# Kernel tuning notes

Measured on AMD Instinct MI355X. Metric: run time of the kernel, lower is better.

Reference implementation:

```python
import jax, jax.numpy as jnp
import numpy as np

EPS = 1e-12   # F.normalize eps
COS_EPS = 1e-8  # F.cosine_similarity eps

B, S, V, D, P, L = 4, 2048, 64, 1024, 8, 24
H = D // 24            # prefix_transform bottleneck = 42
K = 2 * L * D          # 49152 output feature dim


def setup_inputs() -> dict:
    key = jax.random.key(0)
    ks = jax.random.split(key, 8)
    return {
        "prefix": jax.random.randint(ks[0], (B, V), 0, V),
        "ctx_embeds": jax.random.normal(ks[1], (B, S, D), jnp.float32),
        "tables": jax.random.normal(ks[2], (P, V, D), jnp.float32) * 0.02,
        "lora_prefix_emb": jax.random.normal(ks[3], (P, D), jnp.float32),
        "w1": jax.random.normal(ks[4], (D, H), jnp.float32) * 0.02,
        "b1": jnp.zeros((H,), jnp.float32),
        "w2": jax.random.normal(ks[5], (H, K), jnp.float32) * 0.02,
        "b2": jnp.zeros((K,), jnp.float32),
    }


def _gates(ctx_embeds, lora_prefix_emb):
    """select_prefix, vectorized over the num_prefix_set loop.

    The original builds sim_i = bmm(norm(emb), norm(e_i.repeat(B,S,1), dim=0).permute)
    of shape [B,S,S]; since the key is repeated, every column of sim is identical,
    so we carry the column vector [P,B,S] and the math is exact.
    """
    b, s, _ = ctx_embeds.shape
    # normalize embedding over feature dim (F.normalize p=2 dim=2)
    emb_n = ctx_embeds / jnp.maximum(
        jnp.linalg.norm(ctx_embeds, axis=2, keepdims=True), EPS)
    # F.normalize over dim=0 of a tensor repeated B times -> sign(x)/sqrt(B)
    u = lora_prefix_emb / jnp.maximum(
        jnp.sqrt(float(b)) * jnp.abs(lora_prefix_emb), EPS)  # [P,D]
    v = jnp.einsum('bsd,pd->pbs', emb_n, u)          # column of sim matrix
    c = jnp.maximum(v, 0.0)                          # clamp(min=0)
    # F.normalize over last dim (length S, all entries equal c) -> c/(sqrt(S)*c)
    n = c / jnp.maximum(jnp.sqrt(float(s)) * c, EPS)
    w = jax.nn.softmax(n, axis=2)                    # softmax over token dim (dim=1 in torch layout)
    a_v = jnp.einsum('pbs,bsd->pbd', w, ctx_embeds)  # attended value per expert
    e_norm = jnp.linalg.norm(lora_prefix_emb, axis=1)          # [P]
    a_norm = jnp.linalg.norm(a_v, axis=2)                      # [P,B]
    cos = jnp.einsum('pd,pbd->pb', lora_prefix_emb, a_v) / \
        jnp.maximum(e_norm[:, None] * a_norm, COS_EPS)
    return jax.nn.softmax(cos.T, axis=-1)            # self.s_t, [B,P]


def reference(prefix, ctx_embeds, tables, lora_prefix_emb, w1, b1, w2, b2):
    s_t = _gates(ctx_embeds, lora_prefix_emb)        # [B,P]
    # forward() re-applies softmax to self.s_t (faithful double softmax)
    gate = jax.nn.softmax(s_t, axis=-1)              # [B,P]
    tok = tables[:, prefix]                          # [P,B,V,D] per-expert embedding lookup
    h = jnp.tanh(jnp.einsum('pbvd,dh->pbvh', tok, w1) + b1)
    pkv = jnp.einsum('pbvh,hk->pbvk', h, w2) + b2    # [P,B,V,K]
    out = jnp.einsum('bp,pbvk->bvk', gate, pkv)      # gated mixture over experts
    return out
```

## Files before the change

### kernel.cpp

```cpp
#include <hip/hip_runtime.h>

#define BB 4
#define SS 2048
#define VV 64
#define DD 1024
#define PP 8
#define HH 42
#define KK 49152

static constexpr float F_EPS = 1e-12f;
static constexpr float ALPHA = 1.02234304f;

__global__ __launch_bounds__(512) void kU_fused(
    const float* __restrict__ ctx, const float* __restrict__ lora,
    const float* __restrict__ tables, const float* __restrict__ w1,
    const float* __restrict__ b1, float* __restrict__ part,
    float* __restrict__ h_all) {
  __shared__ float smem[PP * DD + 16 + 32 * PP];
  const int t = threadIdx.x;
  const int b = blockIdx.y;
  if (blockIdx.x < 64) {
    const int chunk = blockIdx.x;
    float* u_lds = smem;
    float* w_lds = smem + PP * DD + 16;
    for (int i = t; i < PP * DD; i += 512) {
      float e = lora[i];
      u_lds[i] = e / fmaxf(2.0f * fabsf(e), F_EPS);
    }
    __syncthreads();
    const int wave = t >> 6, lane = t & 63;
    const int rbase = b * SS + chunk * 32 + wave * 4;
    const float4* ctx4 = (const float4*)ctx;
    const float4* u4 = (const float4*)u_lds;
    float dot[4][PP];
    #pragma unroll
    for (int i = 0; i < 4; ++i)
      #pragma unroll
      for (int p = 0; p < PP; ++p) dot[i][p] = 0.f;
    #pragma unroll
    for (int j = 0; j < 4; ++j) {
      float4 c[4];
      #pragma unroll
      for (int i = 0; i < 4; ++i)
        c[i] = ctx4[(size_t)(rbase + i) * 256 + j * 64 + lane];
      #pragma unroll
      for (int p = 0; p < PP; ++p) {
        float4 u = u4[p * 256 + j * 64 + lane];
        #pragma unroll
        for (int i = 0; i < 4; ++i)
          dot[i][p] += c[i].x * u.x + c[i].y * u.y + c[i].z * u.z + c[i].w * u.w;
      }
    }
    const int sel = lane & 7;
    #pragma unroll
    for (int i = 0; i < 4; ++i) {
      float d0 = dot[i][0], d1 = dot[i][1], d2 = dot[i][2], d3 = dot[i][3];
      float d4 = dot[i][4], d5 = dot[i][5], d6 = dot[i][6], d7 = dot[i][7];
      #pragma unroll
      for (int m = 1; m <= 4; m <<= 1) {
        d0 += __shfl_xor(d0, m, 64); d1 += __shfl_xor(d1, m, 64);
        d2 += __shfl_xor(d2, m, 64); d3 += __shfl_xor(d3, m, 64);
        d4 += __shfl_xor(d4, m, 64); d5 += __shfl_xor(d5, m, 64);
        d6 += __shfl_xor(d6, m, 64); d7 += __shfl_xor(d7, m, 64);
      }
      float v = d0;
      v = (sel == 1) ? d1 : v; v = (sel == 2) ? d2 : v;
      v = (sel == 3) ? d3 : v; v = (sel == 4) ? d4 : v;
      v = (sel == 5) ? d5 : v; v = (sel == 6) ? d6 : v;
      v = (sel == 7) ? d7 : v;
      v += __shfl_xor(v, 8, 64);
      v += __shfl_xor(v, 16, 64);
      v += __shfl_xor(v, 32, 64);
      if (lane < PP)
        w_lds[(wave * 4 + i) * PP + lane] = (v > 0.0f) ? ALPHA : 1.0f;
    }
    __syncthreads();
    float2 acc[PP];
    #pragma unroll
    for (int p = 0; p < PP; ++p) acc[p] = make_float2(0.f, 0.f);
    const float2* ctx2 = (const float2*)ctx;
    const float4* w4 = (const float4*)w_lds;
    #pragma unroll 4
    for (int sl = 0; sl < 32; ++sl) {
      float2 c = ctx2[(size_t)(b * SS + chunk * 32 + sl) * 512 + t];
      float4 wa = w4[sl * 2];
      float4 wb = w4[sl * 2 + 1];
      float w[PP] = {wa.x, wa.y, wa.z, wa.w, wb.x, wb.y, wb.z, wb.w};
      #pragma unroll
      for (int p = 0; p < PP; ++p) {
        acc[p].x += w[p] * c.x;
        acc[p].y += w[p] * c.y;
      }
    }
    float2* part2 = (float2*)part;
    #pragma unroll
    for (int p = 0; p < PP; ++p)
      part2[(size_t)((b * 64 + chunk) * PP + p) * 512 + t] = acc[p];
  } else {
    float* row_lds = smem;
    float* partial = smem + DD;
    const int r = (blockIdx.x - 64) * 4 + b;
    ((float2*)row_lds)[t] = ((const float2*)(tables + (size_t)r * DD))[t];
    __syncthreads();
    const int h = t & 63, q = t >> 6;
    float acc = 0.0f;
    if (h < HH) {
      const int d0 = q * 128;
      #pragma unroll 8
      for (int dl = 0; dl < 128; ++dl) {
        acc += row_lds[d0 + dl] * w1[(size_t)(d0 + dl) * HH + h];
      }
    }
    partial[q * 64 + h] = acc;
    __syncthreads();
    if (t < HH) {
      float s = 0.0f;
      #pragma unroll
      for (int q8 = 0; q8 < 8; ++q8) s += partial[q8 * 64 + t];
      h_all[(size_t)r * HH + t] = tanhf(s + b1[t]);
    }
  }
}

__global__ __launch_bounds__(256) void k4_cos(
    const float* __restrict__ part, const float* __restrict__ lora,
    float* __restrict__ cos_ws) {
  const int t = threadIdx.x;
  const int p = blockIdx.x, b = blockIdx.y;
  const float4* part4 = (const float4*)part;
  float4 av = make_float4(0.f, 0.f, 0.f, 0.f);
  #pragma unroll 8
  for (int c = 0; c < 64; ++c) {
    float4 x = part4[(size_t)((b * 64 + c) * PP + p) * 256 + t];
    av.x += x.x; av.y += x.y; av.z += x.z; av.w += x.w;
  }
  float4 e = ((const float4*)lora)[p * 256 + t];
  float dt = av.x * e.x + av.y * e.y + av.z * e.z + av.w * e.w;
  float a2 = av.x * av.x + av.y * av.y + av.z * av.z + av.w * av.w;
  float e2 = e.x * e.x + e.y * e.y + e.z * e.z + e.w * e.w;
  #pragma unroll
  for (int m = 32; m >= 1; m >>= 1) {
    dt += __shfl_xor(dt, m, 64);
    a2 += __shfl_xor(a2, m, 64);
    e2 += __shfl_xor(e2, m, 64);
  }
  __shared__ float red[4][3];
  const int wave = t >> 6, lane = t & 63;
  if (lane == 0) { red[wave][0] = dt; red[wave][1] = a2; red[wave][2] = e2; }
  __syncthreads();
  if (t == 0) {
    float Dv = red[0][0] + red[1][0] + red[2][0] + red[3][0];
    float Av = red[0][1] + red[1][1] + red[2][1] + red[3][1];
    float Ev = red[0][2] + red[1][2] + red[2][2] + red[3][2];
    cos_ws[b * PP + p] = Dv / fmaxf(sqrtf(Ev) * sqrtf(Av), 1e-8f);
  }
}

__global__ __launch_bounds__(256) void k7_out(
    const float* __restrict__ w2, const float* __restrict__ b2,
    const float* __restrict__ h_all, const float* __restrict__ cos_ws,
    const int* __restrict__ prefix, float* __restrict__ out) {
  __shared__ float gate_lds[PP];
  __shared__ float hg_lds[HH * 64];
  __shared__ float w2_lds[HH * 128];
  const int t = threadIdx.x;
  const int b = blockIdx.y;
  const size_t kbase = (size_t)blockIdx.x * 128;
  for (int i = t; i < HH * 128; i += 256) {
    int h = i >> 7, kk = i & 127;
    w2_lds[i] = w2[(size_t)h * KK + kbase + kk];
  }
  if (t == 0) {
    float c[PP];
    float m = -1e30f;
    #pragma unroll
    for (int p = 0; p < PP; ++p) { c[p] = cos_ws[b * PP + p]; m = fmaxf(m, c[p]); }
    float s = 0.0f;
    #pragma unroll
    for (int p = 0; p < PP; ++p) { c[p] = expf(c[p] - m); s += c[p]; }
    float inv = 1.0f / s;
    float m2 = -1e30f;
    #pragma unroll
    for (int p = 0; p < PP; ++p) { c[p] *= inv; m2 = fmaxf(m2, c[p]); }
    float s2 = 0.0f;
    #pragma unroll
    for (int p = 0; p < PP; ++p) { c[p] = expf(c[p] - m2); s2 += c[p]; }
    float inv2 = 1.0f / s2;
    #pragma unroll
    for (int p = 0; p < PP; ++p) gate_lds[p] = c[p] * inv2;
  }
  __syncthreads();
  for (int idx = t; idx < 64 * HH; idx += 256) {
    int v = idx / HH;
    int h = idx - v * HH;
    int tokv = prefix[b * VV + v];
    float s = 0.0f;
    #pragma unroll
    for (int p = 0; p < PP; ++p)
      s += gate_lds[p] * h_all[(size_t)(p * VV + tokv) * HH + h];
    hg_lds[h * 64 + v] = s;
  }
  __syncthreads();
  const int tk = t & 31, tb = t >> 5;
  float4 acc[8];
  #pragma unroll
  for (int i = 0; i < 8; ++i) acc[i] = make_float4(0.f, 0.f, 0.f, 0.f);
  const float4* w24 = (const float4*)w2_lds;
  const float4* hg4 = (const float4*)hg_lds;
  #pragma unroll 2
  for (int h = 0; h < HH; ++h) {
    float4 wv = w24[h * 32 + tk];
    float4 g0 = hg4[h * 16 + tb * 2];
    float4 g1 = hg4[h * 16 + tb * 2 + 1];
    float gg[8] = {g0.x, g0.y, g0.z, g0.w, g1.x, g1.y, g1.z, g1.w};
    #pragma unroll
    for (int i = 0; i < 8; ++i) {
      acc[i].x += gg[i] * wv.x;
      acc[i].y += gg[i] * wv.y;
      acc[i].z += gg[i] * wv.z;
      acc[i].w += gg[i] * wv.w;
    }
  }
  float4 b2v = ((const float4*)b2)[(kbase >> 2) + tk];
  float4* out4 = (float4*)out;
  #pragma unroll
  for (int i = 0; i < 8; ++i) {
    int bv = b * 64 + tb * 8 + i;
    float4 o;
    o.x = acc[i].x + b2v.x;
    o.y = acc[i].y + b2v.y;
    o.z = acc[i].z + b2v.z;
    o.w = acc[i].w + b2v.w;
    out4[(((size_t)bv * KK + kbase) >> 2) + tk] = o;
  }
}

extern "C" void kernel_launch(void* const* d_in, const int* in_sizes, int n_in,
                              void* d_out, int out_size, void* d_ws, size_t ws_size,
                              hipStream_t stream) {
  const int* prefix = (const int*)d_in[0];
  const float* ctx = (const float*)d_in[1];
  const float* tables = (const float*)d_in[2];
  const float* lora = (const float*)d_in[3];
  const float* w1 = (const float*)d_in[4];
  const float* b1 = (const float*)d_in[5];
  const float* w2 = (const float*)d_in[6];
  const float* b2 = (const float*)d_in[7];
  float* out = (float*)d_out;
  char* ws = (char*)d_ws;
  float* part = (float*)ws;
  float* cos_ws = (float*)(ws + 8388608);
  float* h_all = (float*)(ws + 8388608 + 128);

  kU_fused<<<dim3(192, 4), 512, 0, stream>>>(ctx, lora, tables, w1, b1, part, h_all);
  k4_cos<<<dim3(8, 4), 256, 0, stream>>>(part, lora, cos_ws);
  k7_out<<<dim3(384, 4), 256, 0, stream>>>(w2, b2, h_all, cos_ws, prefix, out);
}
```

Before: 152.7 us.

## Process two batches per block in output kernel to reuse staged w2 tile

The output kernel now handles two batch rows per block, halving grid.y. Each staged w2 slice in LDS then serves both batches, which halves the global reads of w2. Each thread now computes 8x8 outputs across two float4 columns. This doubles accumulator registers and halves the block count, which may reduce occupancy and parallelism. The output writes per thread become two adjacent float4 stores.

```diff
diff --git a/kernel.cpp b/kernel.cpp
--- a/kernel.cpp
+++ b/kernel.cpp
@@ -160,17 +160,18 @@
     const float* __restrict__ w2, const float* __restrict__ b2,
     const float* __restrict__ h_all, const float* __restrict__ cos_ws,
     const int* __restrict__ prefix, float* __restrict__ out) {
-  __shared__ float gate_lds[PP];
-  __shared__ float hg_lds[HH * 64];
+  __shared__ float gate_lds[2][PP];
+  __shared__ float hg_lds[2][HH * 64];
   __shared__ float w2_lds[HH * 128];
   const int t = threadIdx.x;
-  const int b = blockIdx.y;
+  const int bp = blockIdx.y;
   const size_t kbase = (size_t)blockIdx.x * 128;
   for (int i = t; i < HH * 128; i += 256) {
     int h = i >> 7, kk = i & 127;
     w2_lds[i] = w2[(size_t)h * KK + kbase + kk];
   }
-  if (t == 0) {
+  if (t < 2) {
+    const int b = bp * 2 + t;
     float c[PP];
     float m = -1e30f;
     #pragma unroll
@@ -187,51 +188,69 @@
     for (int p = 0; p < PP; ++p) { c[p] = expf(c[p] - m2); s2 += c[p]; }
     float inv2 = 1.0f / s2;
     #pragma unroll
-    for (int p = 0; p < PP; ++p) gate_lds[p] = c[p] * inv2;
+    for (int p = 0; p < PP; ++p) gate_lds[t][p] = c[p] * inv2;
   }
   __syncthreads();
-  for (int idx = t; idx < 64 * HH; idx += 256) {
-    int v = idx / HH;
-    int h = idx - v * HH;
-    int tokv = prefix[b * VV + v];
+  for (int idx = t; idx < 2 * 64 * HH; idx += 256) {
+    int bsel = (idx >= 64 * HH) ? 1 : 0;
+    int local = idx - bsel * (64 * HH);
+    int v = local & 63;
+    int h = local >> 6;
+    int tokv = prefix[(bp * 2 + bsel) * VV + v];
     float s = 0.0f;
     #pragma unroll
     for (int p = 0; p < PP; ++p)
-      s += gate_lds[p] * h_all[(size_t)(p * VV + tokv) * HH + h];
-    hg_lds[h * 64 + v] = s;
+      s += gate_lds[bsel][p] * h_all[(size_t)(p * VV + tokv) * HH + h];
+    hg_lds[bsel][h * 64 + v] = s;
   }
   __syncthreads();
-  const int tk = t & 31, tb = t >> 5;
-  float4 acc[8];
+  const int tkg = t & 15;
+  const int tbg = t >> 4;
+  const int bsel = tbg >> 3;
+  const int v0 = (tbg & 7) * 8;
+  float4 acc[8][2];
   #pragma unroll
-  for (int i = 0; i < 8; ++i) acc[i] = make_float4(0.f, 0.f, 0.f, 0.f);
+  for (int i = 0; i < 8; ++i) {
+    acc[i][0] = make_float4(0.f, 0.f, 0.f, 0.f);
+    acc[i][1] = make_float4(0.f, 0.f, 0.f, 0.f);
+  }
   const float4* w24 = (const float4*)w2_lds;
-  const float4* hg4 = (const float4*)hg_lds;
+  const float4* hg4 = (const float4*)hg_lds[bsel];
   #pragma unroll 2
   for (int h = 0; h < HH; ++h) {
-    float4 wv = w24[h * 32 + tk];
-    float4 g0 = hg4[h * 16 + tb * 2];
-    float4 g1 = hg4[h * 16 + tb * 2 + 1];
+    float4 w0 = w24[h * 32 + tkg * 2];
+    float4 w1v = w24[h * 32 + tkg * 2 + 1];
+    float4 g0 = hg4[h * 16 + (v0 >> 2)];
+    float4 g1 = hg4[h * 16 + (v0 >> 2) + 1];
     float gg[8] = {g0.x, g0.y, g0.z, g0.w, g1.x, g1.y, g1.z, g1.w};
     #pragma unroll
     for (int i = 0; i < 8; ++i) {
-      acc[i].x += gg[i] * wv.x;
-      acc[i].y += gg[i] * wv.y;
-      acc[i].z += gg[i] * wv.z;
-      acc[i].w += gg[i] * wv.w;
-    }
-  }
-  float4 b2v = ((const float4*)b2)[(kbase >> 2) + tk];
+      acc[i][0].x += gg[i] * w0.x;
+      acc[i][0].y += gg[i] * w0.y;
+      acc[i][0].z += gg[i] * w0.z;
+      acc[i][0].w += gg[i] * w0.w;
+      acc[i][1].x += gg[i] * w1v.x;
+      acc[i][1].y += gg[i] * w1v.y;
+      acc[i][1].z += gg[i] * w1v.z;
+      acc[i][1].w += gg[i] * w1v.w;
+    }
+  }
+  const float4* b24 = (const float4*)b2;
+  float4 b2a = b24[(kbase >> 2) + tkg * 2];
+  float4 b2b = b24[(kbase >> 2) + tkg * 2 + 1];
   float4* out4 = (float4*)out;
+  const int b = bp * 2 + bsel;
   #pragma unroll
   for (int i = 0; i < 8; ++i) {
-    int bv = b * 64 + tb * 8 + i;
-    float4 o;
-    o.x = acc[i].x + b2v.x;
-    o.y = acc[i].y + b2v.y;
-    o.z = acc[i].z + b2v.z;
-    o.w = acc[i].w + b2v.w;
-    out4[(((size_t)bv * KK + kbase) >> 2) + tk] = o;
+    int bv = b * 64 + v0 + i;
+    size_t base = (((size_t)bv * KK + kbase) >> 2) + tkg * 2;
+    float4 o0, o1;
+    o0.x = acc[i][0].x + b2a.x; o0.y = acc[i][0].y + b2a.y;
+    o0.z = acc[i][0].z + b2a.z; o0.w = acc[i][0].w + b2a.w;
+    o1.x = acc[i][1].x + b2b.x; o1.y = acc[i][1].y + b2b.y;
+    o1.z = acc[i][1].z + b2b.z; o1.w = acc[i][1].w + b2b.w;
+    out4[base] = o0;
+    out4[base + 1] = o1;
   }
 }
 
@@ -254,5 +273,5 @@
 
   kU_fused<<<dim3(192, 4), 512, 0, stream>>>(ctx, lora, tables, w1, b1, part, h_all);
   k4_cos<<<dim3(8, 4), 256, 0, stream>>>(part, lora, cos_ws);
-  k7_out<<<dim3(384, 4), 256, 0, stream>>>(w2, b2, h_all, cos_ws, prefix, out);
-}
+  k7_out<<<dim3(384, 2), 256, 0, stream>>>(w2, b2, h_all, cos_ws, prefix, out);
+}
```

After: 184.6 us. 1.21x slower.
